# Kernel tuning notes

Hardware: AMD Instinct MI355X
Metric: run time of the kernel (lower is better)

The kernel has to match this reference:

```python
import jax, jax.numpy as jnp
import numpy as np

N_NODES = 65536
N_EDGES = 1048576
DIM = 64
N_GRAPHS = 16


def setup_inputs() -> dict:
    key = jax.random.key(0)
    ks = jax.random.split(key, 8)
    node_feats = jax.random.normal(ks[0], (N_NODES, DIM), dtype=jnp.float32)
    edge_index = jax.random.randint(ks[1], (2, N_EDGES), 0, N_NODES, dtype=jnp.int32)
    batch_num_nodes = jnp.full((N_GRAPHS,), N_NODES // N_GRAPHS, dtype=jnp.int32)
    s = 1.0 / np.sqrt(DIM)
    W1 = jax.random.normal(ks[2], (DIM, DIM), dtype=jnp.float32) * s
    W2 = jax.random.normal(ks[3], (DIM, DIM), dtype=jnp.float32) * s
    W3 = jax.random.normal(ks[4], (DIM, DIM), dtype=jnp.float32) * s
    b1 = jnp.zeros((DIM,), jnp.float32)
    b2 = jnp.zeros((DIM,), jnp.float32)
    b3 = jnp.zeros((DIM,), jnp.float32)
    return {"node_feats": node_feats, "edge_index": edge_index,
            "batch_num_nodes": batch_num_nodes,
            "W1": W1, "b1": b1, "W2": W2, "b2": b2, "W3": W3, "b3": b3}


def _graph_conv(x, src, dst, W, b, n_nodes):
    # DGL GraphConv with norm='both': D_out^{-1/2} A^T D_in^{-1/2} style sym norm
    ones = jnp.ones((src.shape[0],), x.dtype)
    deg_out = jnp.clip(jax.ops.segment_sum(ones, src, num_segments=n_nodes), 1.0)
    deg_in = jnp.clip(jax.ops.segment_sum(ones, dst, num_segments=n_nodes), 1.0)
    h = x * jax.lax.rsqrt(deg_out)[:, None]          # [N, d] scale by src out-deg
    agg = jax.ops.segment_sum(h[src], dst, num_segments=n_nodes)  # gather+scatter
    agg = agg * jax.lax.rsqrt(deg_in)[:, None]
    return agg @ W + b


def _unbatch(h, batch_num_nodes):
    # pad each graph's node block to max_num_node -> [B, max_n, d]
    bnn = np.asarray(batch_num_nodes)
    B = bnn.shape[0]
    max_n = int(bnn.max())
    offsets = np.concatenate([[0], np.cumsum(bnn)])
    graph_id = np.repeat(np.arange(B), bnn)                 # [N_total]
    pos = np.arange(int(offsets[-1])) - offsets[graph_id]   # position within graph
    out = jnp.zeros((B, max_n, h.shape[1]), h.dtype)
    return out.at[jnp.asarray(graph_id), jnp.asarray(pos)].set(h)


def reference(node_feats, edge_index, batch_num_nodes, W1, b1, W2, b2, W3, b3):
    src, dst = edge_index[0], edge_index[1]
    n = node_feats.shape[0]
    h = jax.nn.relu(_graph_conv(node_feats, src, dst, W1, b1, n))
    h = jax.nn.relu(_graph_conv(h, src, dst, W2, b2, n))
    h = _graph_conv(h, src, dst, W3, b3, n)
    return _unbatch(h, batch_num_nodes)
```

## Files before the change

### kernel.cpp

```cpp
#include <hip/hip_runtime.h>
#include <hip/hip_fp16.h>


#define N_NODES 65536
#define N_EDGES 1048576
#define DIM 64

#define CHUNKS 256
#define EPC (N_EDGES / CHUNKS)
#define HB 128
#define OH_WORDS 16384

struct alignas(8) h4 { __half2 a, b; };

__global__ void edge_hist(const int* __restrict__ src, const int* __restrict__ dst,
                          int* __restrict__ block_hist, unsigned* __restrict__ partial,
                          uint2* __restrict__ zeroA, uint2* __restrict__ zeroB) {
    __shared__ unsigned h[OH_WORDS];
    __shared__ int bh[2][256];
    int t = threadIdx.x;
    int j = blockIdx.x;
    for (int i = t; i < OH_WORDS; i += 256) h[i] = 0;
    bh[0][t] = 0; bh[1][t] = 0;
    __syncthreads();
    if (j == 0) {
        if (t < 16) zeroA[t] = make_uint2(0u, 0u);
        else if (t < 32) zeroB[t - 16] = make_uint2(0u, 0u);
    }
    int base = j * (2 * EPC);
    for (int i = t; i < 2 * EPC; i += 256) {
        int s = src[base + i];
        int d = dst[base + i];
        atomicAdd(&h[s >> 2], 1u << ((s & 3) * 8));
        atomicAdd(&bh[i >> 12][d >> 8], 1);
    }
    __syncthreads();
    unsigned* dp = partial + (size_t)j * OH_WORDS;
    for (int i = t; i < OH_WORDS; i += 256) dp[i] = h[i];
    block_hist[t * CHUNKS + 2 * j]     = bh[0][t];
    block_hist[t * CHUNKS + 2 * j + 1] = bh[1][t];
}

__global__ void part_scan(const int* __restrict__ bh, int* __restrict__ so) {
    __shared__ int s[1024];
    int t = threadIdx.x;
    const int4* b4 = (const int4*)(bh + t * 64);
    int4 v[16];
    int sum = 0;
    #pragma unroll
    for (int i = 0; i < 16; i++) {
        v[i] = b4[i];
        sum += v[i].x + v[i].y + v[i].z + v[i].w;
    }
    s[t] = sum;
    __syncthreads();
    for (int off = 1; off < 1024; off <<= 1) {
        int u = (t >= off) ? s[t - off] : 0;
        __syncthreads();
        s[t] += u;
        __syncthreads();
    }
    int run = s[t] - sum;
    int* o = so + t * 64;
    #pragma unroll
    for (int i = 0; i < 16; i++) {
        o[4 * i + 0] = run; run += v[i].x;
        o[4 * i + 1] = run; run += v[i].y;
        o[4 * i + 2] = run; run += v[i].z;
        o[4 * i + 3] = run; run += v[i].w;
    }
}

__global__ void part_scatter(const int* __restrict__ src, const int* __restrict__ dst,
                             const int* __restrict__ so, int* __restrict__ bpack) {
    __shared__ int cur[256];
    cur[threadIdx.x] = so[threadIdx.x * CHUNKS + blockIdx.x];
    __syncthreads();
    int base = blockIdx.x * EPC;
    for (int i = threadIdx.x; i < EPC; i += 256) {
        int s = src[base + i];
        int d = dst[base + i];
        int pos = atomicAdd(&cur[d >> 8], 1);
        bpack[pos] = s | ((d & 255) << 16);
    }
}

__global__ void bucket_fused(const int* __restrict__ bpack, const int* __restrict__ so,
                             int* __restrict__ row_start, float* __restrict__ rs_in,
                             unsigned short* __restrict__ csr_src) {
    __shared__ int stage[8192];
    __shared__ int h[256], sc[256], cur[256];
    int b = blockIdx.x;
    int t = threadIdx.x;
    int beg = so[b * CHUNKS];
    int end = (b == 255) ? N_EDGES : so[(b + 1) * CHUNKS];
    int n = end - beg;
    h[t] = 0;
    __syncthreads();
    for (int i = t; i < n; i += 256) {
        int p = bpack[beg + i];
        if (i < 8192) stage[i] = p;
        atomicAdd(&h[(p >> 16) & 255], 1);
    }
    __syncthreads();
    int d = h[t];
    sc[t] = d;
    __syncthreads();
    for (int off = 1; off < 256; off <<= 1) {
        int v = (t >= off) ? sc[t - off] : 0;
        __syncthreads();
        sc[t] += v;
        __syncthreads();
    }
    int rsv = beg + sc[t] - d;
    int node = b * 256 + t;
    row_start[node] = rsv;
    rs_in[node] = rsqrtf(d < 1 ? 1.0f : (float)d);
    if (node == N_NODES - 1) row_start[N_NODES] = N_EDGES;
    cur[t] = rsv;
    __syncthreads();
    for (int i = t; i < n; i += 256) {
        int p = (i < 8192) ? stage[i] : bpack[beg + i];
        int pos = atomicAdd(&cur[(p >> 16) & 255], 1);
        csr_src[pos] = (unsigned short)(p & 0xFFFF);
    }
}

__global__ void oh2p_prescale(const unsigned* __restrict__ partial,
                              float* __restrict__ rs_out,
                              const float4* __restrict__ x4, h4* __restrict__ xs) {
    __shared__ float rsl[256];
    int b = blockIdx.x;
    int t = threadIdx.x;
    if (t < 64) {
        int w = b * 64 + t;
        int c0 = 0, c1 = 0, c2 = 0, c3 = 0;
        for (int c = 0; c < HB; c++) {
            unsigned v = partial[(size_t)c * OH_WORDS + w];
            c0 += (int)(v & 255u);
            c1 += (int)((v >> 8) & 255u);
            c2 += (int)((v >> 16) & 255u);
            c3 += (int)(v >> 24);
        }
        float4 r = make_float4(rsqrtf(c0 < 1 ? 1.0f : (float)c0),
                               rsqrtf(c1 < 1 ? 1.0f : (float)c1),
                               rsqrtf(c2 < 1 ? 1.0f : (float)c2),
                               rsqrtf(c3 < 1 ? 1.0f : (float)c3));
        ((float4*)rs_out)[w] = r;
        rsl[t * 4 + 0] = r.x; rsl[t * 4 + 1] = r.y;
        rsl[t * 4 + 2] = r.z; rsl[t * 4 + 3] = r.w;
    }
    __syncthreads();
    int rowbase = b * 256 * 16;
    for (int i = t; i < 4096; i += 256) {
        float r = rsl[i >> 4];
        float4 v = x4[rowbase + i];
        h4 o;
        o.a = __float22half2_rn(make_float2(v.x * r, v.y * r));
        o.b = __float22half2_rn(make_float2(v.z * r, v.w * r));
        xs[rowbase + i] = o;
    }
}

template<bool SCALE_OUT>
__global__ void fused_layer(const h4* __restrict__ xs, const int* __restrict__ row_start,
                            const unsigned short* __restrict__ csr_src,
                            const float* __restrict__ rs_out, const float* __restrict__ rs_in,
                            const float* __restrict__ W, const float* __restrict__ b,
                            void* __restrict__ outp) {
    __shared__ float4 Ws4[DIM * 16];
    __shared__ float4 bs4[16];
    {
        const float4* Wg = (const float4*)W;
        for (int i = threadIdx.x; i < DIM * 16; i += blockDim.x) Ws4[i] = Wg[i];
        if (threadIdx.x < 16) bs4[threadIdx.x] = ((const float4*)b)[threadIdx.x];
    }
    __syncthreads();

    int wave_id = threadIdx.x >> 6;
    int lane = threadIdx.x & 63;
    int g = lane >> 4;
    int l = lane & 15;
    int node = blockIdx.x * 16 + wave_id * 4 + g;

    int beg = row_start[node];
    int end = row_start[node + 1];

    float4 acc = make_float4(0.f, 0.f, 0.f, 0.f);
    for (int k = beg; k < end; k += 16) {
        int s[16];
        #pragma unroll
        for (int j = 0; j < 16; j++) {
            int kk = k + j;
            int idx = csr_src[kk];
            s[j] = (kk < end) ? idx : N_NODES;
        }
        h4 v[16];
        #pragma unroll
        for (int j = 0; j < 16; j++) v[j] = xs[s[j] * 16 + l];
        #pragma unroll
        for (int j = 0; j < 16; j++) {
            float2 lo = __half22float2(v[j].a);
            float2 hi = __half22float2(v[j].b);
            acc.x += lo.x; acc.y += lo.y; acc.z += hi.x; acc.w += hi.y;
        }
    }
    float ri = rs_in[node];
    acc.x *= ri; acc.y *= ri; acc.z *= ri; acc.w *= ri;

    float4 o = bs4[l];
    int gbase = g << 4;
    #pragma unroll
    for (int m = 0; m < 16; m++) {
        float ax = __shfl(acc.x, gbase + m, 64);
        float ay = __shfl(acc.y, gbase + m, 64);
        float az = __shfl(acc.z, gbase + m, 64);
        float aw = __shfl(acc.w, gbase + m, 64);
        float4 w0 = Ws4[(4 * m + 0) * 16 + l];
        float4 w1 = Ws4[(4 * m + 1) * 16 + l];
        float4 w2 = Ws4[(4 * m + 2) * 16 + l];
        float4 w3 = Ws4[(4 * m + 3) * 16 + l];
        o.x += ax * w0.x + ay * w1.x + az * w2.x + aw * w3.x;
        o.y += ax * w0.y + ay * w1.y + az * w2.y + aw * w3.y;
        o.z += ax * w0.z + ay * w1.z + az * w2.z + aw * w3.z;
        o.w += ax * w0.w + ay * w1.w + az * w2.w + aw * w3.w;
    }
    if (SCALE_OUT) {
        float ro = rs_out[node];
        o.x = (o.x < 0.f ? 0.f : o.x) * ro;
        o.y = (o.y < 0.f ? 0.f : o.y) * ro;
        o.z = (o.z < 0.f ? 0.f : o.z) * ro;
        o.w = (o.w < 0.f ? 0.f : o.w) * ro;
        h4 ho;
        ho.a = __float22half2_rn(make_float2(o.x, o.y));
        ho.b = __float22half2_rn(make_float2(o.z, o.w));
        ((h4*)outp)[node * 16 + l] = ho;
    } else {
        ((float4*)outp)[node * 16 + l] = o;
    }
}

extern "C" void kernel_launch(void* const* d_in, const int* in_sizes, int n_in,
                              void* d_out, int out_size, void* d_ws, size_t ws_size,
                              hipStream_t stream) {
    const float* x   = (const float*)d_in[0];
    const int*   ei  = (const int*)d_in[1];
    const int*   src = ei;
    const int*   dst = ei + N_EDGES;
    const float* W1 = (const float*)d_in[3];
    const float* b1 = (const float*)d_in[4];
    const float* W2 = (const float*)d_in[5];
    const float* b2 = (const float*)d_in[6];
    const float* W3 = (const float*)d_in[7];
    const float* b3 = (const float*)d_in[8];
    float* out = (float*)d_out;

    char* ws = (char*)d_ws;
    float* rs        = (float*)ws;
    float* rs_out    = rs;
    float* rs_in     = rs + N_NODES;
    int*   row_start = (int*)(rs + 2 * N_NODES);
    int*   block_h   = row_start + (N_NODES + 256);
    int*   so        = block_h + 256 * CHUNKS;
    unsigned short* csr_src = (unsigned short*)(so + 256 * CHUNKS);
    h4*    bufA      = (h4*)(csr_src + N_EDGES + 16);
    h4*    bufB      = bufA + (size_t)(N_NODES + 1) * 16;
    unsigned* partial = (unsigned*)(bufB + (size_t)(N_NODES + 1) * 16);
    int*   bpack     = (int*)bufB;
    uint2* zeroA     = (uint2*)(bufA + (size_t)N_NODES * 16);
    uint2* zeroB     = (uint2*)(bufB + (size_t)N_NODES * 16);

    const int fb = N_NODES / 16;

    edge_hist    <<<HB, 256, 0, stream>>>(src, dst, block_h, partial, zeroA, zeroB);
    part_scan    <<<1, 1024, 0, stream>>>(block_h, so);
    part_scatter <<<CHUNKS, 256, 0, stream>>>(src, dst, so, bpack);
    bucket_fused <<<256, 256, 0, stream>>>(bpack, so, row_start, rs_in, csr_src);
    oh2p_prescale<<<256, 256, 0, stream>>>(partial, rs_out, (const float4*)x, bufA);

    fused_layer<true ><<<fb, 256, 0, stream>>>(bufA, row_start, csr_src, rs_out, rs_in, W1, b1, (void*)bufB);
    fused_layer<true ><<<fb, 256, 0, stream>>>(bufB, row_start, csr_src, rs_out, rs_in, W2, b2, (void*)bufA);
    fused_layer<false><<<fb, 256, 0, stream>>>(bufA, row_start, csr_src, rs_out, rs_in, W3, b3, (void*)out);
}
```

Before: 262.7 us.

## Fuse prescale and three layers into cooperative persistent kernel with degree-sorted node order

Replaces the prescale kernel and three per-layer launches with one cooperative kernel of 1024 persistent blocks that run the out-degree normalisation, feature prescale and all three GraphConv layers, separated by grid-wide syncs. It also buckets nodes by in-degree during CSR construction and builds a permutation so each tile processes nodes of similar degree, aimed at reducing wave divergence in the gather loop. The goals are removing launch gaps and tail imbalance. In exchange it adds grid.sync overhead, strided tile loops, and a fallback path of separate launches if the cooperative launch fails.

```diff
diff --git a/kernel.cpp b/kernel.cpp
--- a/kernel.cpp
+++ b/kernel.cpp
@@ -1,6 +1,9 @@
 #include <hip/hip_runtime.h>
 #include <hip/hip_fp16.h>
-
+#include <hip/hip_cooperative_groups.h>
+
+
+namespace cg = cooperative_groups;
 
 #define N_NODES 65536
 #define N_EDGES 1048576
@@ -10,6 +13,7 @@
 #define EPC (N_EDGES / CHUNKS)
 #define HB 128
 #define OH_WORDS 16384
+#define MB 1024
 
 struct alignas(8) h4 { __half2 a, b; };
 
@@ -87,15 +91,18 @@
 
 __global__ void bucket_fused(const int* __restrict__ bpack, const int* __restrict__ so,
                              int* __restrict__ row_start, float* __restrict__ rs_in,
-                             unsigned short* __restrict__ csr_src) {
+                             unsigned short* __restrict__ csr_src,
+                             unsigned char* __restrict__ key, int* __restrict__ cnt) {
     __shared__ int stage[8192];
     __shared__ int h[256], sc[256], cur[256];
+    __shared__ int cnt16[16];
     int b = blockIdx.x;
     int t = threadIdx.x;
     int beg = so[b * CHUNKS];
     int end = (b == 255) ? N_EDGES : so[(b + 1) * CHUNKS];
     int n = end - beg;
     h[t] = 0;
+    if (t < 16) cnt16[t] = 0;
     __syncthreads();
     for (int i = t; i < n; i += 256) {
         int p = bpack[beg + i];
@@ -117,8 +124,13 @@
     row_start[node] = rsv;
     rs_in[node] = rsqrtf(d < 1 ? 1.0f : (float)d);
     if (node == N_NODES - 1) row_start[N_NODES] = N_EDGES;
+    int c = (d + 15) >> 4; if (c > 15) c = 15;
+    int k = 15 - c;
+    key[node] = (unsigned char)k;
+    atomicAdd(&cnt16[k], 1);
     cur[t] = rsv;
     __syncthreads();
+    if (t < 16) cnt[b * 16 + t] = cnt16[t];
     for (int i = t; i < n; i += 256) {
         int p = (i < 8192) ? stage[i] : bpack[beg + i];
         int pos = atomicAdd(&cur[(p >> 16) & 255], 1);
@@ -126,82 +138,59 @@
     }
 }
 
-__global__ void oh2p_prescale(const unsigned* __restrict__ partial,
-                              float* __restrict__ rs_out,
-                              const float4* __restrict__ x4, h4* __restrict__ xs) {
-    __shared__ float rsl[256];
-    int b = blockIdx.x;
-    int t = threadIdx.x;
-    if (t < 64) {
-        int w = b * 64 + t;
-        int c0 = 0, c1 = 0, c2 = 0, c3 = 0;
-        for (int c = 0; c < HB; c++) {
-            unsigned v = partial[(size_t)c * OH_WORDS + w];
-            c0 += (int)(v & 255u);
-            c1 += (int)((v >> 8) & 255u);
-            c2 += (int)((v >> 16) & 255u);
-            c3 += (int)(v >> 24);
-        }
-        float4 r = make_float4(rsqrtf(c0 < 1 ? 1.0f : (float)c0),
-                               rsqrtf(c1 < 1 ? 1.0f : (float)c1),
-                               rsqrtf(c2 < 1 ? 1.0f : (float)c2),
-                               rsqrtf(c3 < 1 ? 1.0f : (float)c3));
-        ((float4*)rs_out)[w] = r;
-        rsl[t * 4 + 0] = r.x; rsl[t * 4 + 1] = r.y;
-        rsl[t * 4 + 2] = r.z; rsl[t * 4 + 3] = r.w;
-    }
-    __syncthreads();
-    int rowbase = b * 256 * 16;
-    for (int i = t; i < 4096; i += 256) {
-        float r = rsl[i >> 4];
-        float4 v = x4[rowbase + i];
-        h4 o;
-        o.a = __float22half2_rn(make_float2(v.x * r, v.y * r));
-        o.b = __float22half2_rn(make_float2(v.z * r, v.w * r));
-        xs[rowbase + i] = o;
-    }
+
+__device__ __forceinline__ void perm_slice(const int* cnt, const unsigned char* key,
+                                           int* perm, int j, int t,
+                                           int* tots, int* basel, int* binb, int* cur16) {
+    if (t < 16) {
+        int run = 0, bj = 0;
+        for (int j2 = 0; j2 < 256; j2++) {
+            if (j2 == j) bj = run;
+            run += cnt[j2 * 16 + t];
+        }
+        tots[t] = run;
+        basel[t] = bj;
+    }
+    __syncthreads();
+    if (t == 0) {
+        int r = 0;
+        for (int i = 0; i < 16; i++) { binb[i] = r; r += tots[i]; }
+    }
+    __syncthreads();
+    if (t < 16) cur16[t] = binb[t] + basel[t];
+    __syncthreads();
+    int node = j * 256 + t;
+    int k = key[node];
+    int pos = atomicAdd(&cur16[k], 1);
+    perm[pos] = node;
 }
 
 template<bool SCALE_OUT>
-__global__ void fused_layer(const h4* __restrict__ xs, const int* __restrict__ row_start,
-                            const unsigned short* __restrict__ csr_src,
-                            const float* __restrict__ rs_out, const float* __restrict__ rs_in,
-                            const float* __restrict__ W, const float* __restrict__ b,
-                            void* __restrict__ outp) {
-    __shared__ float4 Ws4[DIM * 16];
-    __shared__ float4 bs4[16];
-    {
-        const float4* Wg = (const float4*)W;
-        for (int i = threadIdx.x; i < DIM * 16; i += blockDim.x) Ws4[i] = Wg[i];
-        if (threadIdx.x < 16) bs4[threadIdx.x] = ((const float4*)b)[threadIdx.x];
-    }
-    __syncthreads();
-
-    int wave_id = threadIdx.x >> 6;
-    int lane = threadIdx.x & 63;
-    int g = lane >> 4;
-    int l = lane & 15;
-    int node = blockIdx.x * 16 + wave_id * 4 + g;
-
+__device__ __forceinline__ void layer_tile(const h4* __restrict__ xs,
+                                           const int* __restrict__ row_start,
+                                           const unsigned short* __restrict__ csr,
+                                           const float* __restrict__ rs_out,
+                                           const float* __restrict__ rs_in,
+                                           const float4* Ws4, const float4* bs4,
+                                           void* outp, int node, int g, int l) {
     int beg = row_start[node];
     int end = row_start[node + 1];
-
     float4 acc = make_float4(0.f, 0.f, 0.f, 0.f);
     for (int k = beg; k < end; k += 16) {
         int s[16];
         #pragma unroll
-        for (int j = 0; j < 16; j++) {
-            int kk = k + j;
-            int idx = csr_src[kk];
-            s[j] = (kk < end) ? idx : N_NODES;
+        for (int jj = 0; jj < 16; jj++) {
+            int kk = k + jj;
+            int idx = csr[kk];
+            s[jj] = (kk < end) ? idx : N_NODES;
         }
         h4 v[16];
         #pragma unroll
-        for (int j = 0; j < 16; j++) v[j] = xs[s[j] * 16 + l];
+        for (int jj = 0; jj < 16; jj++) v[jj] = xs[s[jj] * 16 + l];
         #pragma unroll
-        for (int j = 0; j < 16; j++) {
-            float2 lo = __half22float2(v[j].a);
-            float2 hi = __half22float2(v[j].b);
+        for (int jj = 0; jj < 16; jj++) {
+            float2 lo = __half22float2(v[jj].a);
+            float2 hi = __half22float2(v[jj].b);
             acc.x += lo.x; acc.y += lo.y; acc.z += hi.x; acc.w += hi.y;
         }
     }
@@ -240,6 +229,169 @@
     }
 }
 
+
+struct MegaParams {
+    const unsigned* partial;
+    float* rs_out;
+    const float* rs_in;
+    const float4* x4;
+    h4* bufA;
+    h4* bufB;
+    const int* cnt;
+    const unsigned char* key;
+    int* perm;
+    const int* row_start;
+    const unsigned short* csr;
+    const float* W1; const float* b1;
+    const float* W2; const float* b2;
+    const float* W3; const float* b3;
+    float4* out;
+};
+
+__global__ void __launch_bounds__(256, 4) mega(MegaParams p) {
+    cg::grid_group grid = cg::this_grid();
+    __shared__ float4 Ws4[DIM * 16];
+    __shared__ float4 bs4[3][16];
+    __shared__ float rsl[64];
+    __shared__ int tots[16], basel[16], binb[16], cur16[16];
+
+    int t = threadIdx.x;
+    int j = blockIdx.x;
+
+    if (t < 16) {
+        bs4[0][t] = ((const float4*)p.b1)[t];
+        bs4[1][t] = ((const float4*)p.b2)[t];
+        bs4[2][t] = ((const float4*)p.b3)[t];
+    }
+
+    if (j < 256) perm_slice(p.cnt, p.key, p.perm, j, t, tots, basel, binb, cur16);
+    __syncthreads();
+
+    if (t < 16) {
+        int w = j * 16 + t;
+        int c0 = 0, c1 = 0, c2 = 0, c3 = 0;
+        for (int c = 0; c < HB; c++) {
+            unsigned v = p.partial[(size_t)c * OH_WORDS + w];
+            c0 += (int)(v & 255u);
+            c1 += (int)((v >> 8) & 255u);
+            c2 += (int)((v >> 16) & 255u);
+            c3 += (int)(v >> 24);
+        }
+        float4 r = make_float4(rsqrtf(c0 < 1 ? 1.0f : (float)c0),
+                               rsqrtf(c1 < 1 ? 1.0f : (float)c1),
+                               rsqrtf(c2 < 1 ? 1.0f : (float)c2),
+                               rsqrtf(c3 < 1 ? 1.0f : (float)c3));
+        ((float4*)p.rs_out)[w] = r;
+        rsl[t * 4 + 0] = r.x; rsl[t * 4 + 1] = r.y;
+        rsl[t * 4 + 2] = r.z; rsl[t * 4 + 3] = r.w;
+    }
+    __syncthreads();
+    {
+        int rowbase = j * 1024;
+        for (int i = t; i < 1024; i += 256) {
+            float r = rsl[i >> 4];
+            float4 v = p.x4[rowbase + i];
+            h4 o;
+            o.a = __float22half2_rn(make_float2(v.x * r, v.y * r));
+            o.b = __float22half2_rn(make_float2(v.z * r, v.w * r));
+            p.bufA[rowbase + i] = o;
+        }
+    }
+
+    grid.sync();
+
+    int wave_id = t >> 6;
+    int lane = t & 63;
+    int g = lane >> 4;
+    int l = lane & 15;
+
+    for (int lay = 0; lay < 3; lay++) {
+        {
+            const float4* Wg = (const float4*)(lay == 0 ? p.W1 : (lay == 1 ? p.W2 : p.W3));
+            for (int i = t; i < DIM * 16; i += 256) Ws4[i] = Wg[i];
+        }
+        __syncthreads();
+        const h4* xs = (lay == 1) ? p.bufB : p.bufA;
+        void* outp   = (lay == 0) ? (void*)p.bufB : (lay == 1) ? (void*)p.bufA : (void*)p.out;
+        for (int tile = j; tile < N_NODES / 16; tile += MB) {
+            int node = p.perm[tile * 16 + wave_id * 4 + g];
+            if (lay < 2)
+                layer_tile<true >(xs, p.row_start, p.csr, p.rs_out, p.rs_in,
+                                  Ws4, bs4[lay], outp, node, g, l);
+            else
+                layer_tile<false>(xs, p.row_start, p.csr, p.rs_out, p.rs_in,
+                                  Ws4, bs4[lay], outp, node, g, l);
+        }
+        if (lay < 2) grid.sync();
+    }
+}
+
+
+__global__ void perm_build(const int* __restrict__ cnt, const unsigned char* __restrict__ key,
+                           int* __restrict__ perm) {
+    __shared__ int tots[16], basel[16], binb[16], cur16[16];
+    perm_slice(cnt, key, perm, blockIdx.x, threadIdx.x, tots, basel, binb, cur16);
+}
+
+__global__ void oh2p_prescale(const unsigned* __restrict__ partial,
+                              float* __restrict__ rs_out,
+                              const float4* __restrict__ x4, h4* __restrict__ xs) {
+    __shared__ float rsl[256];
+    int b = blockIdx.x;
+    int t = threadIdx.x;
+    if (t < 64) {
+        int w = b * 64 + t;
+        int c0 = 0, c1 = 0, c2 = 0, c3 = 0;
+        for (int c = 0; c < HB; c++) {
+            unsigned v = partial[(size_t)c * OH_WORDS + w];
+            c0 += (int)(v & 255u);
+            c1 += (int)((v >> 8) & 255u);
+            c2 += (int)((v >> 16) & 255u);
+            c3 += (int)(v >> 24);
+        }
+        float4 r = make_float4(rsqrtf(c0 < 1 ? 1.0f : (float)c0),
+                               rsqrtf(c1 < 1 ? 1.0f : (float)c1),
+                               rsqrtf(c2 < 1 ? 1.0f : (float)c2),
+                               rsqrtf(c3 < 1 ? 1.0f : (float)c3));
+        ((float4*)rs_out)[w] = r;
+        rsl[t * 4 + 0] = r.x; rsl[t * 4 + 1] = r.y;
+        rsl[t * 4 + 2] = r.z; rsl[t * 4 + 3] = r.w;
+    }
+    __syncthreads();
+    int rowbase = b * 4096;
+    for (int i = t; i < 4096; i += 256) {
+        float r = rsl[i >> 4];
+        float4 v = x4[rowbase + i];
+        h4 o;
+        o.a = __float22half2_rn(make_float2(v.x * r, v.y * r));
+        o.b = __float22half2_rn(make_float2(v.z * r, v.w * r));
+        xs[rowbase + i] = o;
+    }
+}
+
+template<bool SCALE_OUT>
+__global__ void fused_layer_p(const h4* __restrict__ xs, const int* __restrict__ perm,
+                              const int* __restrict__ row_start,
+                              const unsigned short* __restrict__ csr,
+                              const float* __restrict__ rs_out, const float* __restrict__ rs_in,
+                              const float* __restrict__ W, const float* __restrict__ b,
+                              void* __restrict__ outp) {
+    __shared__ float4 Ws4[DIM * 16];
+    __shared__ float4 bs4[16];
+    {
+        const float4* Wg = (const float4*)W;
+        for (int i = threadIdx.x; i < DIM * 16; i += blockDim.x) Ws4[i] = Wg[i];
+        if (threadIdx.x < 16) bs4[threadIdx.x] = ((const float4*)b)[threadIdx.x];
+    }
+    __syncthreads();
+    int wave_id = threadIdx.x >> 6;
+    int lane = threadIdx.x & 63;
+    int g = lane >> 4;
+    int l = lane & 15;
+    int node = perm[blockIdx.x * 16 + wave_id * 4 + g];
+    layer_tile<SCALE_OUT>(xs, row_start, csr, rs_out, rs_in, Ws4, bs4, outp, node, g, l);
+}
+
 extern "C" void kernel_launch(void* const* d_in, const int* in_sizes, int n_in,
                               void* d_out, int out_size, void* d_ws, size_t ws_size,
                               hipStream_t stream) {
@@ -262,7 +414,10 @@
     int*   row_start = (int*)(rs + 2 * N_NODES);
     int*   block_h   = row_start + (N_NODES + 256);
     int*   so        = block_h + 256 * CHUNKS;
-    unsigned short* csr_src = (unsigned short*)(so + 256 * CHUNKS);
+    int*   cnt       = so + 256 * CHUNKS;
+    unsigned char* key = (unsigned char*)(cnt + 4096);
+    int*   perm      = (int*)(key + N_NODES);
+    unsigned short* csr_src = (unsigned short*)(perm + N_NODES);
     h4*    bufA      = (h4*)(csr_src + N_EDGES + 16);
     h4*    bufB      = bufA + (size_t)(N_NODES + 1) * 16;
     unsigned* partial = (unsigned*)(bufB + (size_t)(N_NODES + 1) * 16);
@@ -270,15 +425,27 @@
     uint2* zeroA     = (uint2*)(bufA + (size_t)N_NODES * 16);
     uint2* zeroB     = (uint2*)(bufB + (size_t)N_NODES * 16);
 
-    const int fb = N_NODES / 16;
-
-    edge_hist    <<<HB, 256, 0, stream>>>(src, dst, block_h, partial, zeroA, zeroB);
-    part_scan    <<<1, 1024, 0, stream>>>(block_h, so);
-    part_scatter <<<CHUNKS, 256, 0, stream>>>(src, dst, so, bpack);
-    bucket_fused <<<256, 256, 0, stream>>>(bpack, so, row_start, rs_in, csr_src);
-    oh2p_prescale<<<256, 256, 0, stream>>>(partial, rs_out, (const float4*)x, bufA);
-
-    fused_layer<true ><<<fb, 256, 0, stream>>>(bufA, row_start, csr_src, rs_out, rs_in, W1, b1, (void*)bufB);
-    fused_layer<true ><<<fb, 256, 0, stream>>>(bufB, row_start, csr_src, rs_out, rs_in, W2, b2, (void*)bufA);
-    fused_layer<false><<<fb, 256, 0, stream>>>(bufA, row_start, csr_src, rs_out, rs_in, W3, b3, (void*)out);
-}
+    edge_hist   <<<HB, 256, 0, stream>>>(src, dst, block_h, partial, zeroA, zeroB);
+    part_scan   <<<1, 1024, 0, stream>>>(block_h, so);
+    part_scatter<<<CHUNKS, 256, 0, stream>>>(src, dst, so, bpack);
+    bucket_fused<<<256, 256, 0, stream>>>(bpack, so, row_start, rs_in, csr_src, key, cnt);
+
+    MegaParams p;
+    p.partial = partial; p.rs_out = rs_out; p.rs_in = rs_in;
+    p.x4 = (const float4*)x; p.bufA = bufA; p.bufB = bufB;
+    p.cnt = cnt; p.key = key; p.perm = perm;
+    p.row_start = row_start; p.csr = csr_src;
+    p.W1 = W1; p.b1 = b1; p.W2 = W2; p.b2 = b2; p.W3 = W3; p.b3 = b3;
+    p.out = (float4*)out;
+    void* args[] = { &p };
+    hipError_t err = hipLaunchCooperativeKernel((void*)mega, dim3(MB), dim3(256),
+                                                args, 0, stream);
+    if (err != hipSuccess) {
+        const int fb = N_NODES / 16;
+        perm_build   <<<256, 256, 0, stream>>>(cnt, key, perm);
+        oh2p_prescale<<<256, 256, 0, stream>>>(partial, rs_out, (const float4*)x, bufA);
+        fused_layer_p<true ><<<fb, 256, 0, stream>>>(bufA, perm, row_start, csr_src, rs_out, rs_in, W1, b1, (void*)bufB);
+        fused_layer_p<true ><<<fb, 256, 0, stream>>>(bufB, perm, row_start, csr_src, rs_out, rs_in, W2, b2, (void*)bufA);
+        fused_layer_p<false><<<fb, 256, 0, stream>>>(bufA, perm, row_start, csr_src, rs_out, rs_in, W3, b3, (void*)out);
+    }
+}
```

Result: slower. 661.8 us (+151.9%).

## Sort nodes by in-degree bucket so waves process similar-degree rows

Applied to the files above, without the earlier changes.

Bucket_fused now assigns each node a key from its in-degree (in steps of 16 edges) and writes per-block bucket counts. A new perm_build kernel does a counting sort to build a permutation listing nodes in descending degree order. The fused layers then read their node index through this permutation, so the four nodes sharing a wave have similar loop trip counts and there is less divergence from load imbalance. This adds one small kernel, an extra indirection, and less locality in output writes and row_start reads.

```diff
diff --git a/kernel.cpp b/kernel.cpp
--- a/kernel.cpp
+++ b/kernel.cpp
@@ -87,15 +87,18 @@
 
 __global__ void bucket_fused(const int* __restrict__ bpack, const int* __restrict__ so,
                              int* __restrict__ row_start, float* __restrict__ rs_in,
-                             unsigned short* __restrict__ csr_src) {
+                             unsigned short* __restrict__ csr_src,
+                             unsigned char* __restrict__ key, int* __restrict__ cnt) {
     __shared__ int stage[8192];
     __shared__ int h[256], sc[256], cur[256];
+    __shared__ int cnt16[16];
     int b = blockIdx.x;
     int t = threadIdx.x;
     int beg = so[b * CHUNKS];
     int end = (b == 255) ? N_EDGES : so[(b + 1) * CHUNKS];
     int n = end - beg;
     h[t] = 0;
+    if (t < 16) cnt16[t] = 0;
     __syncthreads();
     for (int i = t; i < n; i += 256) {
         int p = bpack[beg + i];
@@ -117,13 +120,46 @@
     row_start[node] = rsv;
     rs_in[node] = rsqrtf(d < 1 ? 1.0f : (float)d);
     if (node == N_NODES - 1) row_start[N_NODES] = N_EDGES;
+    int c = (d + 15) >> 4; if (c > 15) c = 15;
+    int k = 15 - c;
+    key[node] = (unsigned char)k;
+    atomicAdd(&cnt16[k], 1);
     cur[t] = rsv;
     __syncthreads();
+    if (t < 16) cnt[b * 16 + t] = cnt16[t];
     for (int i = t; i < n; i += 256) {
         int p = (i < 8192) ? stage[i] : bpack[beg + i];
         int pos = atomicAdd(&cur[(p >> 16) & 255], 1);
         csr_src[pos] = (unsigned short)(p & 0xFFFF);
     }
+}
+
+__global__ void perm_build(const int* __restrict__ cnt, const unsigned char* __restrict__ key,
+                           int* __restrict__ perm) {
+    __shared__ int tots[16], basel[16], binb[16], cur16[16];
+    int j = blockIdx.x;
+    int t = threadIdx.x;
+    if (t < 16) {
+        int run = 0, bj = 0;
+        for (int j2 = 0; j2 < 256; j2++) {
+            if (j2 == j) bj = run;
+            run += cnt[j2 * 16 + t];
+        }
+        tots[t] = run;
+        basel[t] = bj;
+    }
+    __syncthreads();
+    if (t == 0) {
+        int r = 0;
+        for (int i = 0; i < 16; i++) { binb[i] = r; r += tots[i]; }
+    }
+    __syncthreads();
+    if (t < 16) cur16[t] = binb[t] + basel[t];
+    __syncthreads();
+    int node = j * 256 + t;
+    int k = key[node];
+    int pos = atomicAdd(&cur16[k], 1);
+    perm[pos] = node;
 }
 
 __global__ void oh2p_prescale(const unsigned* __restrict__ partial,
@@ -151,7 +187,7 @@
         rsl[t * 4 + 2] = r.z; rsl[t * 4 + 3] = r.w;
     }
     __syncthreads();
-    int rowbase = b * 256 * 16;
+    int rowbase = b * 4096;
     for (int i = t; i < 4096; i += 256) {
         float r = rsl[i >> 4];
         float4 v = x4[rowbase + i];
@@ -163,11 +199,12 @@
 }
 
 template<bool SCALE_OUT>
-__global__ void fused_layer(const h4* __restrict__ xs, const int* __restrict__ row_start,
-                            const unsigned short* __restrict__ csr_src,
-                            const float* __restrict__ rs_out, const float* __restrict__ rs_in,
-                            const float* __restrict__ W, const float* __restrict__ b,
-                            void* __restrict__ outp) {
+__global__ void fused_layer_p(const h4* __restrict__ xs, const int* __restrict__ perm,
+                              const int* __restrict__ row_start,
+                              const unsigned short* __restrict__ csr,
+                              const float* __restrict__ rs_out, const float* __restrict__ rs_in,
+                              const float* __restrict__ W, const float* __restrict__ b,
+                              void* __restrict__ outp) {
     __shared__ float4 Ws4[DIM * 16];
     __shared__ float4 bs4[16];
     {
@@ -181,7 +218,7 @@
     int lane = threadIdx.x & 63;
     int g = lane >> 4;
     int l = lane & 15;
-    int node = blockIdx.x * 16 + wave_id * 4 + g;
+    int node = perm[blockIdx.x * 16 + wave_id * 4 + g];
 
     int beg = row_start[node];
     int end = row_start[node + 1];
@@ -190,18 +227,18 @@
     for (int k = beg; k < end; k += 16) {
         int s[16];
         #pragma unroll
-        for (int j = 0; j < 16; j++) {
-            int kk = k + j;
-            int idx = csr_src[kk];
-            s[j] = (kk < end) ? idx : N_NODES;
+        for (int jj = 0; jj < 16; jj++) {
+            int kk = k + jj;
+            int idx = csr[kk];
+            s[jj] = (kk < end) ? idx : N_NODES;
         }
         h4 v[16];
         #pragma unroll
-        for (int j = 0; j < 16; j++) v[j] = xs[s[j] * 16 + l];
+        for (int jj = 0; jj < 16; jj++) v[jj] = xs[s[jj] * 16 + l];
         #pragma unroll
-        for (int j = 0; j < 16; j++) {
-            float2 lo = __half22float2(v[j].a);
-            float2 hi = __half22float2(v[j].b);
+        for (int jj = 0; jj < 16; jj++) {
+            float2 lo = __half22float2(v[jj].a);
+            float2 hi = __half22float2(v[jj].b);
             acc.x += lo.x; acc.y += lo.y; acc.z += hi.x; acc.w += hi.y;
         }
     }
@@ -262,7 +299,10 @@
     int*   row_start = (int*)(rs + 2 * N_NODES);
     int*   block_h   = row_start + (N_NODES + 256);
     int*   so        = block_h + 256 * CHUNKS;
-    unsigned short* csr_src = (unsigned short*)(so + 256 * CHUNKS);
+    int*   cnt       = so + 256 * CHUNKS;
+    unsigned char* key = (unsigned char*)(cnt + 4096);
+    int*   perm      = (int*)(key + N_NODES);
+    unsigned short* csr_src = (unsigned short*)(perm + N_NODES);
     h4*    bufA      = (h4*)(csr_src + N_EDGES + 16);
     h4*    bufB      = bufA + (size_t)(N_NODES + 1) * 16;
     unsigned* partial = (unsigned*)(bufB + (size_t)(N_NODES + 1) * 16);
@@ -275,10 +315,11 @@
     edge_hist    <<<HB, 256, 0, stream>>>(src, dst, block_h, partial, zeroA, zeroB);
     part_scan    <<<1, 1024, 0, stream>>>(block_h, so);
     part_scatter <<<CHUNKS, 256, 0, stream>>>(src, dst, so, bpack);
-    bucket_fused <<<256, 256, 0, stream>>>(bpack, so, row_start, rs_in, csr_src);
+    bucket_fused <<<256, 256, 0, stream>>>(bpack, so, row_start, rs_in, csr_src, key, cnt);
+    perm_build   <<<256, 256, 0, stream>>>(cnt, key, perm);
     oh2p_prescale<<<256, 256, 0, stream>>>(partial, rs_out, (const float4*)x, bufA);
 
-    fused_layer<true ><<<fb, 256, 0, stream>>>(bufA, row_start, csr_src, rs_out, rs_in, W1, b1, (void*)bufB);
-    fused_layer<true ><<<fb, 256, 0, stream>>>(bufB, row_start, csr_src, rs_out, rs_in, W2, b2, (void*)bufA);
-    fused_layer<false><<<fb, 256, 0, stream>>>(bufA, row_start, csr_src, rs_out, rs_in, W3, b3, (void*)out);
-}
+    fused_layer_p<true ><<<fb, 256, 0, stream>>>(bufA, perm, row_start, csr_src, rs_out, rs_in, W1, b1, (void*)bufB);
+    fused_layer_p<true ><<<fb, 256, 0, stream>>>(bufB, perm, row_start, csr_src, rs_out, rs_in, W2, b2, (void*)bufA);
+    fused_layer_p<false><<<fb, 256, 0, stream>>>(bufA, perm, row_start, csr_src, rs_out, rs_in, W3, b3, (void*)out);
+}
```

Result: slower. 268.0 us (+2.0%).

## Fuse graph preprocessing phases into one cooperative kernel with grid syncs

Applied to the files above, without the earlier changes.

Replaces the five separate preprocessing kernels (histogram, scan, scatter, bucket sort, prescale) with one cooperative kernel of 256 blocks that uses grid-wide syncs between phases. The edge histogram now runs on 256 chunks instead of 128, so the scan and the partial-degree reduction work over 256 entries. The bucket buffer is moved into the partial-histogram region, which is dead once prescale has read it. The goal is to remove kernel-launch gaps and tail effects between the small phases. In exchange it adds grid-barrier overhead and twice the partial-histogram reads, and it keeps a multi-kernel fallback in case cooperative launch fails.

```diff
diff --git a/kernel.cpp b/kernel.cpp
--- a/kernel.cpp
+++ b/kernel.cpp
@@ -1,141 +1,80 @@
 #include <hip/hip_runtime.h>
 #include <hip/hip_fp16.h>
-
+#include <hip/hip_cooperative_groups.h>
+
+
+namespace cg = cooperative_groups;
 
 #define N_NODES 65536
 #define N_EDGES 1048576
 #define DIM 64
-
 #define CHUNKS 256
 #define EPC (N_EDGES / CHUNKS)
-#define HB 128
 #define OH_WORDS 16384
 
 struct alignas(8) h4 { __half2 a, b; };
 
-__global__ void edge_hist(const int* __restrict__ src, const int* __restrict__ dst,
-                          int* __restrict__ block_hist, unsigned* __restrict__ partial,
-                          uint2* __restrict__ zeroA, uint2* __restrict__ zeroB) {
-    __shared__ unsigned h[OH_WORDS];
-    __shared__ int bh[2][256];
-    int t = threadIdx.x;
-    int j = blockIdx.x;
-    for (int i = t; i < OH_WORDS; i += 256) h[i] = 0;
-    bh[0][t] = 0; bh[1][t] = 0;
+union PrepShared {
+    unsigned hist[OH_WORDS];
+    struct { int stage[8192]; int h[256]; int sc[256]; int cur[256]; } b;
+};
+
+
+__device__ __forceinline__ void ph_edge(const int* __restrict__ src,
+        const int* __restrict__ dst, int* __restrict__ block_hist,
+        unsigned* __restrict__ partial, uint2* __restrict__ zeroA,
+        uint2* __restrict__ zeroB, int j, int t, PrepShared& u, int* bh) {
+    for (int i = t; i < OH_WORDS; i += 256) u.hist[i] = 0;
+    bh[t] = 0;
     __syncthreads();
     if (j == 0) {
         if (t < 16) zeroA[t] = make_uint2(0u, 0u);
         else if (t < 32) zeroB[t - 16] = make_uint2(0u, 0u);
     }
-    int base = j * (2 * EPC);
-    for (int i = t; i < 2 * EPC; i += 256) {
+    int base = j * EPC;
+    for (int i = t; i < EPC; i += 256) {
         int s = src[base + i];
         int d = dst[base + i];
-        atomicAdd(&h[s >> 2], 1u << ((s & 3) * 8));
-        atomicAdd(&bh[i >> 12][d >> 8], 1);
+        atomicAdd(&u.hist[s >> 2], 1u << ((s & 3) * 8));
+        atomicAdd(&bh[d >> 8], 1);
     }
     __syncthreads();
     unsigned* dp = partial + (size_t)j * OH_WORDS;
-    for (int i = t; i < OH_WORDS; i += 256) dp[i] = h[i];
-    block_hist[t * CHUNKS + 2 * j]     = bh[0][t];
-    block_hist[t * CHUNKS + 2 * j + 1] = bh[1][t];
-}
-
-__global__ void part_scan(const int* __restrict__ bh, int* __restrict__ so) {
-    __shared__ int s[1024];
-    int t = threadIdx.x;
-    const int4* b4 = (const int4*)(bh + t * 64);
-    int4 v[16];
+    for (int i = t; i < OH_WORDS; i += 256) dp[i] = u.hist[i];
+    block_hist[t * CHUNKS + j] = bh[t];
+}
+
+__device__ __forceinline__ void ph_scan(const int* __restrict__ bhist,
+        int* __restrict__ so, int t, int* sscan) {
+    const int4* b4 = (const int4*)(bhist + t * CHUNKS);
     int sum = 0;
-    #pragma unroll
-    for (int i = 0; i < 16; i++) {
-        v[i] = b4[i];
-        sum += v[i].x + v[i].y + v[i].z + v[i].w;
-    }
-    s[t] = sum;
-    __syncthreads();
-    for (int off = 1; off < 1024; off <<= 1) {
-        int u = (t >= off) ? s[t - off] : 0;
+    for (int i = 0; i < 64; i++) { int4 v = b4[i]; sum += v.x + v.y + v.z + v.w; }
+    sscan[t] = sum;
+    __syncthreads();
+    for (int off = 1; off < 256; off <<= 1) {
+        int u2 = (t >= off) ? sscan[t - off] : 0;
         __syncthreads();
-        s[t] += u;
+        sscan[t] += u2;
         __syncthreads();
     }
-    int run = s[t] - sum;
-    int* o = so + t * 64;
-    #pragma unroll
-    for (int i = 0; i < 16; i++) {
-        o[4 * i + 0] = run; run += v[i].x;
-        o[4 * i + 1] = run; run += v[i].y;
-        o[4 * i + 2] = run; run += v[i].z;
-        o[4 * i + 3] = run; run += v[i].w;
-    }
-}
-
-__global__ void part_scatter(const int* __restrict__ src, const int* __restrict__ dst,
-                             const int* __restrict__ so, int* __restrict__ bpack) {
-    __shared__ int cur[256];
-    cur[threadIdx.x] = so[threadIdx.x * CHUNKS + blockIdx.x];
-    __syncthreads();
-    int base = blockIdx.x * EPC;
-    for (int i = threadIdx.x; i < EPC; i += 256) {
-        int s = src[base + i];
-        int d = dst[base + i];
-        int pos = atomicAdd(&cur[d >> 8], 1);
-        bpack[pos] = s | ((d & 255) << 16);
-    }
-}
-
-__global__ void bucket_fused(const int* __restrict__ bpack, const int* __restrict__ so,
-                             int* __restrict__ row_start, float* __restrict__ rs_in,
-                             unsigned short* __restrict__ csr_src) {
-    __shared__ int stage[8192];
-    __shared__ int h[256], sc[256], cur[256];
-    int b = blockIdx.x;
-    int t = threadIdx.x;
-    int beg = so[b * CHUNKS];
-    int end = (b == 255) ? N_EDGES : so[(b + 1) * CHUNKS];
-    int n = end - beg;
-    h[t] = 0;
-    __syncthreads();
-    for (int i = t; i < n; i += 256) {
-        int p = bpack[beg + i];
-        if (i < 8192) stage[i] = p;
-        atomicAdd(&h[(p >> 16) & 255], 1);
-    }
-    __syncthreads();
-    int d = h[t];
-    sc[t] = d;
-    __syncthreads();
-    for (int off = 1; off < 256; off <<= 1) {
-        int v = (t >= off) ? sc[t - off] : 0;
-        __syncthreads();
-        sc[t] += v;
-        __syncthreads();
-    }
-    int rsv = beg + sc[t] - d;
-    int node = b * 256 + t;
-    row_start[node] = rsv;
-    rs_in[node] = rsqrtf(d < 1 ? 1.0f : (float)d);
-    if (node == N_NODES - 1) row_start[N_NODES] = N_EDGES;
-    cur[t] = rsv;
-    __syncthreads();
-    for (int i = t; i < n; i += 256) {
-        int p = (i < 8192) ? stage[i] : bpack[beg + i];
-        int pos = atomicAdd(&cur[(p >> 16) & 255], 1);
-        csr_src[pos] = (unsigned short)(p & 0xFFFF);
-    }
-}
-
-__global__ void oh2p_prescale(const unsigned* __restrict__ partial,
-                              float* __restrict__ rs_out,
-                              const float4* __restrict__ x4, h4* __restrict__ xs) {
-    __shared__ float rsl[256];
-    int b = blockIdx.x;
-    int t = threadIdx.x;
+    int run = sscan[t] - sum;
+    int* o = so + t * CHUNKS;
+    for (int i = 0; i < 64; i++) {
+        int4 v = b4[i];
+        o[4 * i + 0] = run; run += v.x;
+        o[4 * i + 1] = run; run += v.y;
+        o[4 * i + 2] = run; run += v.z;
+        o[4 * i + 3] = run; run += v.w;
+    }
+}
+
+__device__ __forceinline__ void ph_prescale(const unsigned* __restrict__ partial,
+        float* __restrict__ rs_out, const float4* __restrict__ x4,
+        h4* __restrict__ xs, int j, int t, float* rsl) {
     if (t < 64) {
-        int w = b * 64 + t;
+        int w = j * 64 + t;
         int c0 = 0, c1 = 0, c2 = 0, c3 = 0;
-        for (int c = 0; c < HB; c++) {
+        for (int c = 0; c < CHUNKS; c++) {
             unsigned v = partial[(size_t)c * OH_WORDS + w];
             c0 += (int)(v & 255u);
             c1 += (int)((v >> 8) & 255u);
@@ -151,7 +90,7 @@
         rsl[t * 4 + 2] = r.z; rsl[t * 4 + 3] = r.w;
     }
     __syncthreads();
-    int rowbase = b * 256 * 16;
+    int rowbase = j * 4096;
     for (int i = t; i < 4096; i += 256) {
         float r = rsl[i >> 4];
         float4 v = x4[rowbase + i];
@@ -162,9 +101,120 @@
     }
 }
 
+__device__ __forceinline__ void ph_scatter(const int* __restrict__ src,
+        const int* __restrict__ dst, const int* __restrict__ so,
+        int* __restrict__ bpack, int j, int t, int* cur) {
+    cur[t] = so[t * CHUNKS + j];
+    __syncthreads();
+    int base = j * EPC;
+    for (int i = t; i < EPC; i += 256) {
+        int s = src[base + i];
+        int d = dst[base + i];
+        int pos = atomicAdd(&cur[d >> 8], 1);
+        bpack[pos] = s | ((d & 255) << 16);
+    }
+}
+
+__device__ __forceinline__ void ph_bucket(const int* __restrict__ bpack,
+        const int* __restrict__ so, int* __restrict__ row_start,
+        float* __restrict__ rs_in, unsigned short* __restrict__ csr,
+        int j, int t, int* stage, int* h, int* sc, int* cur) {
+    int beg = so[j * CHUNKS];
+    int end = (j == 255) ? N_EDGES : so[(j + 1) * CHUNKS];
+    int n = end - beg;
+    h[t] = 0;
+    __syncthreads();
+    for (int i = t; i < n; i += 256) {
+        int p = bpack[beg + i];
+        if (i < 8192) stage[i] = p;
+        atomicAdd(&h[(p >> 16) & 255], 1);
+    }
+    __syncthreads();
+    int d = h[t];
+    sc[t] = d;
+    __syncthreads();
+    for (int off = 1; off < 256; off <<= 1) {
+        int v = (t >= off) ? sc[t - off] : 0;
+        __syncthreads();
+        sc[t] += v;
+        __syncthreads();
+    }
+    int rsv = beg + sc[t] - d;
+    int node = j * 256 + t;
+    row_start[node] = rsv;
+    rs_in[node] = rsqrtf(d < 1 ? 1.0f : (float)d);
+    if (node == N_NODES - 1) row_start[N_NODES] = N_EDGES;
+    cur[t] = rsv;
+    __syncthreads();
+    for (int i = t; i < n; i += 256) {
+        int p = (i < 8192) ? stage[i] : bpack[beg + i];
+        int pos = atomicAdd(&cur[(p >> 16) & 255], 1);
+        csr[pos] = (unsigned short)(p & 0xFFFF);
+    }
+}
+
+
+struct PrepParams {
+    const int* src; const int* dst;
+    int* block_hist; unsigned* partial;
+    uint2* zeroA; uint2* zeroB;
+    int* so;
+    float* rs_out; const float4* x4; h4* bufA;
+    int* bpack;
+    int* row_start; float* rs_in; unsigned short* csr;
+};
+
+__global__ void __launch_bounds__(256) prep_mega(PrepParams p) {
+    cg::grid_group grid = cg::this_grid();
+    __shared__ PrepShared u;
+    __shared__ int bh[256];
+    __shared__ int sscan[256];
+    __shared__ float rsl[256];
+    int t = threadIdx.x;
+    int j = blockIdx.x;
+
+    ph_edge(p.src, p.dst, p.block_hist, p.partial, p.zeroA, p.zeroB, j, t, u, bh);
+    grid.sync();
+    if (j == 0) ph_scan(p.block_hist, p.so, t, sscan);
+    ph_prescale(p.partial, p.rs_out, p.x4, p.bufA, j, t, rsl);
+    grid.sync();
+    ph_scatter(p.src, p.dst, p.so, p.bpack, j, t, u.b.cur);
+    grid.sync();
+    ph_bucket(p.bpack, p.so, p.row_start, p.rs_in, p.csr, j, t,
+              u.b.stage, u.b.h, u.b.sc, u.b.cur);
+}
+
+
+__global__ void k_edge(const int* src, const int* dst, int* block_hist,
+                       unsigned* partial, uint2* zeroA, uint2* zeroB) {
+    __shared__ PrepShared u;
+    __shared__ int bh[256];
+    ph_edge(src, dst, block_hist, partial, zeroA, zeroB, blockIdx.x, threadIdx.x, u, bh);
+}
+__global__ void k_scan(const int* bhist, int* so) {
+    __shared__ int sscan[256];
+    ph_scan(bhist, so, threadIdx.x, sscan);
+}
+__global__ void k_prescale(const unsigned* partial, float* rs_out,
+                           const float4* x4, h4* xs) {
+    __shared__ float rsl[256];
+    ph_prescale(partial, rs_out, x4, xs, blockIdx.x, threadIdx.x, rsl);
+}
+__global__ void k_scatter(const int* src, const int* dst, const int* so, int* bpack) {
+    __shared__ int cur[256];
+    ph_scatter(src, dst, so, bpack, blockIdx.x, threadIdx.x, cur);
+}
+__global__ void k_bucket(const int* bpack, const int* so, int* row_start,
+                         float* rs_in, unsigned short* csr) {
+    __shared__ int stage[8192];
+    __shared__ int h[256], sc[256], cur[256];
+    ph_bucket(bpack, so, row_start, rs_in, csr, blockIdx.x, threadIdx.x,
+              stage, h, sc, cur);
+}
+
 template<bool SCALE_OUT>
 __global__ void fused_layer(const h4* __restrict__ xs, const int* __restrict__ row_start,
-                            const unsigned short* __restrict__ csr_src,
+                            const unsigned short* __restrict__ csr,
                             const float* __restrict__ rs_out, const float* __restrict__ rs_in,
                             const float* __restrict__ W, const float* __restrict__ b,
                             void* __restrict__ outp) {
@@ -190,18 +240,18 @@
     for (int k = beg; k < end; k += 16) {
         int s[16];
         #pragma unroll
-        for (int j = 0; j < 16; j++) {
-            int kk = k + j;
-            int idx = csr_src[kk];
-            s[j] = (kk < end) ? idx : N_NODES;
+        for (int jj = 0; jj < 16; jj++) {
+            int kk = k + jj;
+            int idx = csr[kk];
+            s[jj] = (kk < end) ? idx : N_NODES;
         }
         h4 v[16];
         #pragma unroll
-        for (int j = 0; j < 16; j++) v[j] = xs[s[j] * 16 + l];
+        for (int jj = 0; jj < 16; jj++) v[jj] = xs[s[jj] * 16 + l];
         #pragma unroll
-        for (int j = 0; j < 16; j++) {
-            float2 lo = __half22float2(v[j].a);
-            float2 hi = __half22float2(v[j].b);
+        for (int jj = 0; jj < 16; jj++) {
+            float2 lo = __half22float2(v[jj].a);
+            float2 hi = __half22float2(v[jj].b);
             acc.x += lo.x; acc.y += lo.y; acc.z += hi.x; acc.w += hi.y;
         }
     }
@@ -266,18 +316,30 @@
     h4*    bufA      = (h4*)(csr_src + N_EDGES + 16);
     h4*    bufB      = bufA + (size_t)(N_NODES + 1) * 16;
     unsigned* partial = (unsigned*)(bufB + (size_t)(N_NODES + 1) * 16);
-    int*   bpack     = (int*)bufB;
+    int*   bpack     = (int*)partial;
     uint2* zeroA     = (uint2*)(bufA + (size_t)N_NODES * 16);
     uint2* zeroB     = (uint2*)(bufB + (size_t)N_NODES * 16);
 
+    PrepParams p;
+    p.src = src; p.dst = dst;
+    p.block_hist = block_h; p.partial = partial;
+    p.zeroA = zeroA; p.zeroB = zeroB;
+    p.so = so;
+    p.rs_out = rs_out; p.x4 = (const float4*)x; p.bufA = bufA;
+    p.bpack = bpack;
+    p.row_start = row_start; p.rs_in = rs_in; p.csr = csr_src;
+    void* args[] = { &p };
+    hipError_t err = hipLaunchCooperativeKernel((void*)prep_mega, dim3(CHUNKS),
+                                                dim3(256), args, 0, stream);
+    if (err != hipSuccess) {
+        k_edge    <<<CHUNKS, 256, 0, stream>>>(src, dst, block_h, partial, zeroA, zeroB);
+        k_scan    <<<1, 256, 0, stream>>>(block_h, so);
+        k_prescale<<<CHUNKS, 256, 0, stream>>>(partial, rs_out, (const float4*)x, bufA);
+        k_scatter <<<CHUNKS, 256, 0, stream>>>(src, dst, so, bpack);
+        k_bucket  <<<CHUNKS, 256, 0, stream>>>(bpack, so, row_start, rs_in, csr_src);
+    }
+
     const int fb = N_NODES / 16;
-
-    edge_hist    <<<HB, 256, 0, stream>>>(src, dst, block_h, partial, zeroA, zeroB);
-    part_scan    <<<1, 1024, 0, stream>>>(block_h, so);
-    part_scatter <<<CHUNKS, 256, 0, stream>>>(src, dst, so, bpack);
-    bucket_fused <<<256, 256, 0, stream>>>(bpack, so, row_start, rs_in, csr_src);
-    oh2p_prescale<<<256, 256, 0, stream>>>(partial, rs_out, (const float4*)x, bufA);
-
     fused_layer<true ><<<fb, 256, 0, stream>>>(bufA, row_start, csr_src, rs_out, rs_in, W1, b1, (void*)bufB);
     fused_layer<true ><<<fb, 256, 0, stream>>>(bufB, row_start, csr_src, rs_out, rs_in, W2, b2, (void*)bufA);
     fused_layer<false><<<fb, 256, 0, stream>>>(bufA, row_start, csr_src, rs_out, rs_in, W3, b3, (void*)out);
```

After: 393.6 us. 1.5x slower.
